# Performance work log

Hardware: AMD Instinct MI355X
Metric: run time of the kernel (lower is better)

Reference implementation:

```python
import jax, jax.numpy as jnp
from jax import lax
import numpy as np

K = 48          # dim_embedding_key
PAST = 20
FUT = 40
N = 65536       # total surrounding-agent nodes
E = 1048576     # edges
B = 1           # batch (structurally forced to 1 by the original code)


def conv1d_relu(x, w, b):
    # x: [B, 2, T], w: [K, 2, 3], padding=1 -> relu(Conv1d)
    y = lax.conv_general_dilated(x, w, (1,), ((1, 1),),
                                 dimension_numbers=('NCH', 'OIH', 'NCH'))
    return jax.nn.relu(y + b[None, :, None])


def gru_cell(xt, h, Wih, Whh, bih, bhh):
    gi = xt @ Wih.T + bih
    gh = h @ Whh.T + bhh
    ir, iz, inn = jnp.split(gi, 3, axis=-1)
    hr, hz, hn = jnp.split(gh, 3, axis=-1)
    r = jax.nn.sigmoid(ir + hr)
    z = jax.nn.sigmoid(iz + hz)
    n = jnp.tanh(inn + r * hn)
    return (1 - z) * n + z * h


def gru_last(x, Wih, Whh, bih, bhh):
    # x: [Nb, T, Din]; returns final hidden state [Nb, H] (torch GRU, h0 = 0)
    h0 = jnp.zeros((x.shape[0], Whh.shape[1]), x.dtype)
    def step(h, xt):
        h2 = gru_cell(xt, h, Wih, Whh, bih, bhh)
        return h2, None
    hT, _ = lax.scan(step, h0, jnp.swapaxes(x, 0, 1))
    return hT


def gcn_conv(x, row, col, w, W, b, n):
    # PyG GCNConv(normalize=True): add self loops (weight 1), symmetric norm,
    # x @ W.T, gather at source `row`, scatter-add at target `col`, + bias.
    loop = jnp.arange(n)
    row = jnp.concatenate([row, loop])
    col = jnp.concatenate([col, loop])
    w = jnp.concatenate([w, jnp.ones((n,), w.dtype)])
    deg = jax.ops.segment_sum(w, col, num_segments=n)
    dinv = jnp.where(deg > 0, lax.rsqrt(jnp.where(deg > 0, deg, 1.0)), 0.0)
    norm = dinv[row] * w * dinv[col]
    xw = x @ W.T
    msg = xw[row] * norm[:, None]
    return jax.ops.segment_sum(msg, col, num_segments=n) + b


def forward(past, future, x, edge_index, edge_weight,
            conv_past_w, conv_past_b, conv_fut_w, conv_fut_b,
            enc_past_Wih, enc_past_Whh, enc_past_bih, enc_past_bhh,
            enc_fut_Wih, enc_fut_Whh, enc_fut_bih, enc_fut_bhh,
            dec_Wih, dec_Whh, dec_bih, dec_bhh,
            fc_w, fc_b, gcn1_w, gcn1_b, gcn2_w, gcn2_b):
    present0 = past[:, -1, :2]                                  # [B, 2]

    # --- surrounding agents: conv1d + GRU encoder over all N nodes ---
    inter_past = jnp.swapaxes(x.reshape(-1, PAST, 2), 1, 2)     # [N, 2, T]
    story_embed = jnp.swapaxes(conv1d_relu(inter_past, conv_past_w, conv_past_b), 1, 2)
    state_past = gru_last(story_embed, enc_past_Wih, enc_past_Whh, enc_past_bih, enc_past_bhh)  # [N, K]

    # --- GCN interaction (edge_weight nonempty branch); dropout is eval-mode identity ---
    ei = edge_index.reshape(2, -1)
    ew = edge_weight.reshape(-1)
    x1 = jax.nn.relu(gcn_conv(state_past, ei[0], ei[1], ew, gcn1_w, gcn1_b, N))
    x1 = gcn_conv(x1, ei[0], ei[1], ew, gcn2_w, gcn2_b, N)
    interact_past = x1[0].reshape(B, -1)                        # [B, K] (B == 1)

    # --- ego past / future encoders ---
    past_embed = jnp.swapaxes(conv1d_relu(jnp.swapaxes(past, 1, 2), conv_past_w, conv_past_b), 1, 2)
    fut_embed = jnp.swapaxes(conv1d_relu(jnp.swapaxes(future, 1, 2), conv_fut_w, conv_fut_b), 1, 2)
    target_past = gru_last(past_embed, enc_past_Wih, enc_past_Whh, enc_past_bih, enc_past_bhh)   # [B, K]
    state_fut = gru_last(fut_embed, enc_fut_Wih, enc_fut_Whh, enc_fut_bih, enc_fut_bhh)          # [B, K]

    state_conc = jnp.concatenate([interact_past, target_past, state_fut], axis=-1)               # [B, 3K]

    zeros_in = jnp.zeros_like(state_conc)
    def step(carry, i):
        h, present = carry
        inp = jnp.where(i == 0, state_conc, zeros_in)
        h = gru_cell(inp, h, dec_Wih, dec_Whh, dec_bih, dec_bhh)
        coords = present + h @ fc_w.T + fc_b
        return (h, coords), coords
    (_, _), coords_seq = lax.scan(step, (jnp.zeros((B, 3 * K), past.dtype), present0), jnp.arange(FUT))
    return jnp.swapaxes(coords_seq, 0, 1)                        # [B, FUT, 2]


def setup_inputs() -> dict:
    ks = jax.random.split(jax.random.key(0), 32)
    def p(k, shape, s=0.1):
        return jax.random.normal(k, shape, jnp.float32) * s
    inp = {
        'past': p(ks[0], (B, PAST, 2), 1.0),
        'future': p(ks[1], (B, FUT, 2), 1.0),
        'x': p(ks[2], (N, PAST, 2), 1.0),
        'edge_index': jax.random.randint(ks[3], (1, 2, E), 0, N, jnp.int32),
        'edge_weight': jax.random.uniform(ks[4], (1, E), jnp.float32),
        'conv_past_w': p(ks[5], (K, 2, 3)), 'conv_past_b': p(ks[6], (K,)),
        'conv_fut_w': p(ks[7], (K, 2, 3)), 'conv_fut_b': p(ks[8], (K,)),
        'enc_past_Wih': p(ks[9], (3 * K, K)), 'enc_past_Whh': p(ks[10], (3 * K, K)),
        'enc_past_bih': p(ks[11], (3 * K,)), 'enc_past_bhh': p(ks[12], (3 * K,)),
        'enc_fut_Wih': p(ks[13], (3 * K, K)), 'enc_fut_Whh': p(ks[14], (3 * K, K)),
        'enc_fut_bih': p(ks[15], (3 * K,)), 'enc_fut_bhh': p(ks[16], (3 * K,)),
        'dec_Wih': p(ks[17], (9 * K, 3 * K)), 'dec_Whh': p(ks[18], (9 * K, 3 * K)),
        'dec_bih': p(ks[19], (9 * K,)), 'dec_bhh': p(ks[20], (9 * K,)),
        'fc_w': p(ks[21], (2, 3 * K)), 'fc_b': p(ks[22], (2,)),
        'gcn1_w': p(ks[23], (K, K)), 'gcn1_b': p(ks[24], (K,)),
        'gcn2_w': p(ks[25], (K, K)), 'gcn2_b': p(ks[26], (K,)),
    }
    return inp


def reference(past, future, x, edge_index, edge_weight,
              conv_past_w, conv_past_b, conv_fut_w, conv_fut_b,
              enc_past_Wih, enc_past_Whh, enc_past_bih, enc_past_bhh,
              enc_fut_Wih, enc_fut_Whh, enc_fut_bih, enc_fut_bhh,
              dec_Wih, dec_Whh, dec_bih, dec_bhh,
              fc_w, fc_b, gcn1_w, gcn1_b, gcn2_w, gcn2_b):
    return forward(past, future, x, edge_index, edge_weight,
                   conv_past_w, conv_past_b, conv_fut_w, conv_fut_b,
                   enc_past_Wih, enc_past_Whh, enc_past_bih, enc_past_bhh,
                   enc_fut_Wih, enc_fut_Whh, enc_fut_bih, enc_fut_bhh,
                   dec_Wih, dec_Whh, dec_bih, dec_bhh,
                   fc_w, fc_b, gcn1_w, gcn1_b, gcn2_w, gcn2_b)
```

## Files before the change

kernel.cpp:

```cpp
#include <hip/hip_runtime.h>
#include <math.h>

#define NN 65536
#define NE 1048576
#define KH 48
#define G3 144
#define DEGB 512
#define PREPB 15

#define CAP_L1 8192
#define CAP_S1 4096
#define CAP_E2 65536
#define CAP_S2 8192

#define OFF_MARK1  0u
#define OFF_MARK2  262144u
#define OFF_CNT    524288u
#define OFF_L1R    524352u
#define OFF_L1W    557120u
#define OFF_S1G    589888u
#define OFF_E2R    606272u
#define OFF_E2S    868416u
#define OFF_E2W    1130560u
#define OFF_S2     1392704u
#define OFF_DEG2   1425472u
#define OFF_STATE  1458240u
#define OFF_X1     3031104u
#define OFF_TPSF   3817536u
#define OFF_WHH16  3818048u
#define OFF_GI0P   3942464u
#define OFF_GIP    3944192u
#define OFF_GIF    3955712u

typedef _Float16 h2_t __attribute__((ext_vector_type(2)));
typedef _Float16 h4_t __attribute__((ext_vector_type(4)));

__device__ __forceinline__ float sigmf(float x) { return 1.0f / (1.0f + expf(-x)); }

#if __has_builtin(__builtin_amdgcn_fdot2)
__device__ __forceinline__ float fdot2f(h2_t a, h2_t b, float c) {
    return __builtin_amdgcn_fdot2(a, b, c, false);
}
#else
__device__ __forceinline__ float fdot2f(h2_t a, h2_t b, float c) {
    return c + (float)a.x * (float)b.x + (float)a.y * (float)b.y;
}
#endif

__global__ void k_edges1(const int* ei, const float* ew,
                         int* mark1, unsigned* cnt, int* l1r, float* l1w,
                         const float* past, const float* future,
                         const float* cpw, const float* cpb,
                         const float* cfw, const float* cfb,
                         const float* epWih, const float* epbih,
                         const float* efWih, const float* efbih,
                         float* giP, float* giF) {
    if (blockIdx.x >= NE / 4 / 256) {
        int p = blockIdx.x - NE / 4 / 256;
        const float* xs; const float* cw; const float* cb;
        const float* Wih; const float* bih; float* gout;
        int T, s0;
        if (p < 5) { xs = past;   cw = cpw; cb = cpb; Wih = epWih; bih = epbih;
                     gout = giP; T = 20; s0 = p * 4; }
        else       { xs = future; cw = cfw; cb = cfb; Wih = efWih; bih = efbih;
                     gout = giF; T = 40; s0 = (p - 5) * 4; }
        __shared__ __align__(16) float s_x[80];
        __shared__ __align__(16) float s_e[4 * KH];
        int t = threadIdx.x;
        if (t < T * 2) s_x[t] = xs[t];
        __syncthreads();
        for (int idx = t; idx < 4 * KH; idx += 256) {
            int lt = idx / KH;
            int k = idx - lt * KH;
            int tt = s0 + lt;
            float acc = cb[k];
#pragma unroll
            for (int d = 0; d < 3; ++d) {
                int tau = tt + d - 1;
                if (tau >= 0 && tau < T) {
                    acc += cw[k * 6 + d] * s_x[tau * 2 + 0];
                    acc += cw[k * 6 + 3 + d] * s_x[tau * 2 + 1];
                }
            }
            s_e[lt * KH + k] = fmaxf(acc, 0.0f);
        }
        __syncthreads();
        for (int idx = t; idx < 4 * G3; idx += 256) {
            int lt = idx / G3;
            int row = idx - lt * G3;
            const float4* wp = reinterpret_cast<const float4*>(Wih + row * KH);
            const float4* em = reinterpret_cast<const float4*>(s_e + lt * KH);
            float g = bih[row];
#pragma unroll
            for (int j = 0; j < 12; ++j) {
                float4 w4 = wp[j]; float4 e4 = em[j];
                g += w4.x * e4.x + w4.y * e4.y + w4.z * e4.z + w4.w * e4.w;
            }
            gout[(s0 + lt) * G3 + row] = g;
        }
        return;
    }
    int q = blockIdx.x * blockDim.x + threadIdx.x;
    if (q >= NE / 4) return;
    if (q == 0) mark1[0] = 1;
    int4 c4 = reinterpret_cast<const int4*>(ei + NE)[q];
    int e = q * 4;
    int cc[4] = {c4.x, c4.y, c4.z, c4.w};
#pragma unroll
    for (int j = 0; j < 4; ++j) {
        if (cc[j] == 0) {
            int r = ei[e + j];
            float w = ew[e + j];
            unsigned s = atomicAdd(&cnt[0], 1u);
            if (s < CAP_L1) { l1r[s] = r; l1w[s] = w; }
            mark1[r] = 1;
        }
    }
}

__global__ void k_compact1(int* mark1, int* mark2, unsigned* cnt,
                           int* e2r, int* e2s, float* e2w, int* s1g,
                           float* x1, const float* g1b) {
    int i = blockIdx.x * blockDim.x + threadIdx.x;
    if (i >= NN) return;
    if (mark1[i]) {
        unsigned s = atomicAdd(&cnt[1], 1u);
        if (s < CAP_S1) {
            mark1[i] = (int)s + 1;
            mark2[i] = 1;
            s1g[s] = i;
            unsigned t = atomicAdd(&cnt[2], 1u);
            if (t < CAP_E2) { e2r[t] = i; e2s[t] = (int)s; e2w[t] = 1.0f; }
            for (int k = 0; k < KH; ++k) x1[s * KH + k] = g1b[k];
        } else {
            mark1[i] = 0;
        }
    }
}

__global__ void k_edges2(const int* ei, const float* ew,
                         const int* mark1, int* mark2, unsigned* cnt,
                         int* e2r, int* e2s, float* e2w) {
    int q = blockIdx.x * blockDim.x + threadIdx.x;
    if (q >= NE / 4) return;
    int4 c4 = reinterpret_cast<const int4*>(ei + NE)[q];
    int e = q * 4;
    int cc[4] = {c4.x, c4.y, c4.z, c4.w};
#pragma unroll
    for (int j = 0; j < 4; ++j) {
        int m = mark1[cc[j]];
        if (m > 0) {
            int r = ei[e + j];
            float w = ew[e + j];
            unsigned s = atomicAdd(&cnt[2], 1u);
            if (s < CAP_E2) { e2r[s] = r; e2s[s] = m - 1; e2w[s] = w; }
            mark2[r] = 1;
        }
    }
}

__global__ void k_compact2(int* mark2, unsigned* cnt, int* s2, float* deg2) {
    int i = blockIdx.x * blockDim.x + threadIdx.x;
    if (i >= NN) return;
    if (mark2[i]) {
        unsigned s = atomicAdd(&cnt[3], 1u);
        if (s < CAP_S2) { s2[s] = i; mark2[i] = (int)s + 1; deg2[s] = 1.0f; }
        else mark2[i] = 0;
    }
}

__device__ void gru_seq(const float* xseq, int T,
                        const float* cw, const float* cb,
                        const float* Wih, const float* Whh,
                        const float* bih, const float* bhh,
                        float* out48,
                        float* s_x, float* s_embed, float* s_giA,
                        float* s_h ) {
    int t = threadIdx.x;
    int nt = blockDim.x;
    for (int i = t; i < T * 2; i += nt) s_x[i] = xseq[i];
    __syncthreads();
    for (int idx = t; idx < T * KH; idx += nt) {
        int tt = idx / KH;
        int k = idx - tt * KH;
        float acc = cb[k];
#pragma unroll
        for (int d = 0; d < 3; ++d) {
            int tau = tt + d - 1;
            if (tau >= 0 && tau < T) {
                acc += cw[k * 6 + d] * s_x[tau * 2 + 0];
                acc += cw[k * 6 + 3 + d] * s_x[tau * 2 + 1];
            }
        }
        s_embed[tt * KH + k] = fmaxf(acc, 0.0f);
    }
    __syncthreads();
    for (int idx = t; idx < T * G3; idx += nt) {
        int step = idx / G3;
        int row = idx - step * G3;
        const float4* wp = reinterpret_cast<const float4*>(Wih + row * KH);
        const float4* em = reinterpret_cast<const float4*>(s_embed + step * KH);
        float g = bih[row];
#pragma unroll
        for (int j = 0; j < 12; ++j) {
            float4 w4 = wp[j]; float4 e4 = em[j];
            g += w4.x * e4.x + w4.y * e4.y + w4.z * e4.z + w4.w * e4.w;
        }
        s_giA[idx] = g;
    }
    int k = t >> 1, hf = t & 1;
    float4 wr[18];
    float bh0 = 0.0f, bh1 = 0.0f, bh2 = 0.0f;
    if (t < 96) {
#pragma unroll
        for (int g = 0; g < 3; ++g) {
            const float4* q = reinterpret_cast<const float4*>(
                Whh + (g * KH + k) * KH + hf * 24);
#pragma unroll
            for (int j = 0; j < 6; ++j) wr[g * 6 + j] = q[j];
        }
        if (hf == 0) { bh0 = bhh[k]; bh1 = bhh[KH + k]; bh2 = bhh[2 * KH + k]; }
    }
    if (t < KH) s_h[t] = 0.0f;
    float hk = 0.0f;
    for (int step = 0; step < T; ++step) {
        __syncthreads();
        int cur = step & 1, nxt = cur ^ 1;
        if (t < 96) {
            const float4* hp = reinterpret_cast<const float4*>(s_h + cur * KH)
                               + hf * 6;
            float a0 = bh0, a1 = bh1, a2 = bh2;
#pragma unroll
            for (int j = 0; j < 6; ++j) {
                float4 hv = hp[j];
                float4 w0 = wr[j], w1 = wr[6 + j], w2 = wr[12 + j];
                a0 += w0.x * hv.x + w0.y * hv.y + w0.z * hv.z + w0.w * hv.w;
                a1 += w1.x * hv.x + w1.y * hv.y + w1.z * hv.z + w1.w * hv.w;
                a2 += w2.x * hv.x + w2.y * hv.y + w2.z * hv.z + w2.w * hv.w;
            }
            a0 += __shfl_xor(a0, 1);
            a1 += __shfl_xor(a1, 1);
            a2 += __shfl_xor(a2, 1);
            if (hf == 0) {
                const float* gi = s_giA + step * G3;
                float r = sigmf(gi[k] + a0);
                float z = sigmf(gi[KH + k] + a1);
                float n = tanhf(gi[2 * KH + k] + r * a2);
                hk = (1.0f - z) * n + z * hk;
                s_h[nxt * KH + k] = hk;
            }
        }
    }
    __syncthreads();
    if (t < KH) out48[t] = s_h[(T & 1) * KH + t];
}

__device__ void gru_rec(const float* giA , int T,
                        const float* Whh, const float* bhh,
                        float* out48, float* s_h ) {
    int t = threadIdx.x;
    int k = t >> 1, hf = t & 1;
    float4 wr[18];
    float bh0 = 0.0f, bh1 = 0.0f, bh2 = 0.0f;
    if (t < 96) {
#pragma unroll
        for (int g = 0; g < 3; ++g) {
            const float4* q = reinterpret_cast<const float4*>(
                Whh + (g * KH + k) * KH + hf * 24);
#pragma unroll
            for (int j = 0; j < 6; ++j) wr[g * 6 + j] = q[j];
        }
        if (hf == 0) { bh0 = bhh[k]; bh1 = bhh[KH + k]; bh2 = bhh[2 * KH + k]; }
    }
    if (t < KH) s_h[t] = 0.0f;
    float hk = 0.0f;
    for (int step = 0; step < T; ++step) {
        __syncthreads();
        int cur = step & 1, nxt = cur ^ 1;
        if (t < 96) {
            const float4* hp = reinterpret_cast<const float4*>(s_h + cur * KH)
                               + hf * 6;
            float a0 = bh0, a1 = bh1, a2 = bh2;
#pragma unroll
            for (int j = 0; j < 6; ++j) {
                float4 hv = hp[j];
                float4 w0 = wr[j], w1 = wr[6 + j], w2 = wr[12 + j];
                a0 += w0.x * hv.x + w0.y * hv.y + w0.z * hv.z + w0.w * hv.w;
                a1 += w1.x * hv.x + w1.y * hv.y + w1.z * hv.z + w1.w * hv.w;
                a2 += w2.x * hv.x + w2.y * hv.y + w2.z * hv.z + w2.w * hv.w;
            }
            a0 += __shfl_xor(a0, 1);
            a1 += __shfl_xor(a1, 1);
            a2 += __shfl_xor(a2, 1);
            if (hf == 0) {
                const float* gi = giA + step * G3;
                float r = sigmf(gi[k] + a0);
                float z = sigmf(gi[KH + k] + a1);
                float n = tanhf(gi[2 * KH + k] + r * a2);
                hk = (1.0f - z) * n + z * hk;
                s_h[nxt * KH + k] = hk;
            }
        }
    }
    __syncthreads();
    if (t < KH) out48[t] = s_h[(T & 1) * KH + t];
}

__global__ __launch_bounds__(192, 2) void k_gru(
    const float* x, const float* cpw, const float* cpb,
    const float* epWih, const float* epWhh, const float* epbih, const float* epbhh,
    const float* efWhh, const float* efbhh,
    const float* giP, const float* giF,
    const int* ei, const float* ew, const int* mark2, float* deg2,
    const int* s2, const unsigned* cnt, float* state, float* tpsf) {
    if (blockIdx.x < DEGB) {
        int per = NE / DEGB;
        int lo = blockIdx.x * per;
        for (int e = lo + threadIdx.x; e < lo + per; e += blockDim.x) {
            int c = ei[NE + e];
            int m = mark2[c];
            if (m > 0) atomicAdd(&deg2[m - 1], ew[e]);
        }
        return;
    }
    __shared__ __align__(16) float s_x[80];
    __shared__ __align__(16) float s_embed[40 * KH];
    __shared__ __align__(16) float s_giA[40 * G3];
    __shared__ __align__(16) float s_h[2 * KH];
    if (blockIdx.x == DEGB) {
        gru_rec(giP, 20, epWhh, epbhh, tpsf, s_h);
        return;
    }
    if (blockIdx.x == DEGB + 1) {
        gru_rec(giF, 40, efWhh, efbhh, tpsf + 64, s_h);
        return;
    }
    int b0 = blockIdx.x - (DEGB + 2);
    int nw = gridDim.x - (DEGB + 2);
    int cnt2 = (int)min(cnt[3], (unsigned)CAP_S2);
    for (int b = b0; b < cnt2; b += nw) {
        int node = s2[b];
        gru_seq(x + (size_t)node * 40, 20, cpw, cpb, epWih, epWhh, epbih, epbhh,
                state + (size_t)b * KH, s_x, s_embed, s_giA, s_h);
    }
}

__global__ void k_acc1(const unsigned* cnt, const int* e2r, const int* e2s,
                       const float* e2w, const int* mark2, const float* deg2,
                       const int* s1g, const float* state,
                       const float* W1, float* x1,
                       const float* dWhh, const float* dWih,
                       const float* dbih, const float* tpsf,
                       _Float16* whh16, float* gi0p) {
    if (blockIdx.x < 64) {
        int id = blockIdx.x * blockDim.x + threadIdx.x;
        if (id < 27 * 576) {
            int c = id / 576, t = id - c * 576;
            int k = t >> 2, q = t & 3;
            int g = c / 9, u = c - g * 9;
            const float* src = dWhh + (size_t)(g * G3 + k) * G3 + q * 36 + 4 * u;
            float4 f = *reinterpret_cast<const float4*>(src);
            h2_t a, b;
            a.x = (_Float16)f.x; a.y = (_Float16)f.y;
            b.x = (_Float16)f.z; b.y = (_Float16)f.w;
            h2_t* o = reinterpret_cast<h2_t*>(whh16);
            o[2 * id + 0] = a;
            o[2 * id + 1] = b;
            return;
        }
        int row = id - 27 * 576;
        if (row < 432) {
            const float* wr = dWih + (size_t)row * G3;
            float acc = dbih[row];
#pragma unroll
            for (int m = 0; m < 48; ++m) acc += wr[48 + m] * tpsf[m];
#pragma unroll
            for (int m = 0; m < 48; ++m) acc += wr[96 + m] * tpsf[64 + m];
            gi0p[row] = acc;
        }
        return;
    }
    int nE = (int)min(cnt[2], (unsigned)CAP_E2);
    int total = nE * KH;
    int stride = (gridDim.x - 64) * blockDim.x;
    for (int idx = (blockIdx.x - 64) * blockDim.x + threadIdx.x; idx < total;
         idx += stride) {
        int e = idx / KH;
        int k = idx - e * KH;
        int row = e2r[e];
        int s2i = mark2[row] - 1;
        if (s2i < 0) continue;
        int cglob = s1g[e2s[e]];
        int cs2 = mark2[cglob] - 1;
        float norm = e2w[e] * rsqrtf(deg2[s2i] * deg2[cs2]);
        const float* sp = state + (size_t)s2i * KH;
        const float* wp = W1 + k * KH;
        float acc = 0.0f;
#pragma unroll
        for (int m = 0; m < KH; ++m) acc += sp[m] * wp[m];
        atomicAdd(&x1[e2s[e] * KH + k], acc * norm);
    }
}

__global__ __launch_bounds__(640, 1) void k_dec(
    const unsigned* cnt, const int* l1r, const float* l1w,
    const int* mark1, const int* mark2, const float* deg2, const float* x1,
    const float* W2, const float* b2, const float* tpsf, const float* past,
    const float* dWih, const _Float16* whh16, const float* gi0p,
    const float* dbih, const float* dbhh,
    const float* fcw, const float* fcb, float* out) {
    __shared__ __align__(16) float s_conc[G3];
    __shared__ __align__(16) _Float16 s_h16[2][G3];
    __shared__ __align__(16) float s_hf[2][G3];
    int t = threadIdx.x;
    if (t < 48) s_conc[t] = b2[t];
    else if (t < 96) s_conc[t] = tpsf[t - 48];
    else if (t < 144) s_conc[t] = tpsf[64 + t - 96];
    if (t < G3) {
        s_h16[0][t] = (_Float16)0.0f;
        s_hf[0][t] = 0.0f;
    }
    __syncthreads();
    int cl1 = (int)min(cnt[0], (unsigned)CAP_L1);
    float dinv0 = rsqrtf(deg2[mark2[0] - 1]);
    int items = (cl1 + 1) * KH;
    for (int idx = t; idx < items; idx += blockDim.x) {
        int e = idx / KH;
        int k = idx - e * KH;
        int row; float norm;
        if (e == cl1) { row = 0; norm = dinv0 * dinv0; }
        else {
            row = l1r[e];
            int rs2 = mark2[row] - 1;
            if (rs2 < 0) continue;
            norm = l1w[e] * rsqrtf(deg2[rs2]) * dinv0;
        }
        int s1 = mark1[row] - 1;
        if (s1 < 0) continue;
        const float* xp = x1 + (size_t)s1 * KH;
        const float* wp = W2 + k * KH;
        float acc = 0.0f;
#pragma unroll
        for (int m = 0; m < KH; ++m) acc += fmaxf(xp[m], 0.0f) * wp[m];
        atomicAdd(&s_conc[k], acc * norm);
    }
    int k = t >> 2, q = t & 3;
    h2_t wh[54];
    float bh[3] = {0.0f, 0.0f, 0.0f};
    float bi[3] = {0.0f, 0.0f, 0.0f};
    if (t < 576) {
        const h4_t* wp = reinterpret_cast<const h4_t*>(whh16);
#pragma unroll
        for (int c = 0; c < 27; ++c) {
            h4_t v = wp[c * 576 + t];
            wh[2 * c] = __builtin_shufflevector(v, v, 0, 1);
            wh[2 * c + 1] = __builtin_shufflevector(v, v, 2, 3);
        }
        if (q == 0) {
#pragma unroll
            for (int g = 0; g < 3; ++g) {
                bh[g] = dbhh[g * G3 + k];
                bi[g] = dbih[g * G3 + k];
            }
        }
    }
    float fw0[3] = {0, 0, 0}, fw1[3] = {0, 0, 0};
    float fcb0 = 0.0f, fcb1 = 0.0f, pres0 = 0.0f, pres1 = 0.0f;
    if (t >= 576) {
        int lane = t - 576;
#pragma unroll
        for (int j = 0; j < 3; ++j) {
            int m = lane + 64 * j;
            if (m < G3) { fw0[j] = fcw[m]; fw1[j] = fcw[G3 + m]; }
        }
        if (lane == 0) {
            fcb0 = fcb[0]; fcb1 = fcb[1];
            pres0 = past[38]; pres1 = past[39];
        }
    }
    __syncthreads();
    float gi0[3] = {0.0f, 0.0f, 0.0f};
    if (t < 576) {
#pragma unroll
        for (int g = 0; g < 3; ++g) {
            float acc = 0.0f;
            if (q == 0) {
                const float4* p = reinterpret_cast<const float4*>(
                    dWih + (size_t)(g * G3 + k) * G3);
                const float4* cc = reinterpret_cast<const float4*>(s_conc);
#pragma unroll
                for (int j = 0; j < 9; ++j) {
                    float4 w4 = p[j]; float4 c4 = cc[j];
                    acc += w4.x * c4.x + w4.y * c4.y + w4.z * c4.z + w4.w * c4.w;
                }
            } else if (q == 1) {
                const float4* p = reinterpret_cast<const float4*>(
                    dWih + (size_t)(g * G3 + k) * G3 + 36);
                const float4* cc = reinterpret_cast<const float4*>(s_conc + 36);
#pragma unroll
                for (int j = 0; j < 3; ++j) {
                    float4 w4 = p[j]; float4 c4 = cc[j];
                    acc += w4.x * c4.x + w4.y * c4.y + w4.z * c4.z + w4.w * c4.w;
                }
            }
            acc += __shfl_xor(acc, 1);
            acc += __shfl_xor(acc, 2);
            gi0[g] = acc + gi0p[g * G3 + k];
        }
    }
    float hk = 0.0f;
    for (int i = 0; i < 40; ++i) {
        __syncthreads();
        int cur = i & 1, nxt = cur ^ 1;
        if (t < 576) {
            const h4_t* hp = reinterpret_cast<const h4_t*>(&s_h16[cur][0]) + q * 9;
            float a0 = bh[0], a1 = bh[1], a2 = bh[2];
#pragma unroll
            for (int j = 0; j < 9; ++j) {
                h4_t hv = hp[j];
                h2_t lo = __builtin_shufflevector(hv, hv, 0, 1);
                h2_t hi = __builtin_shufflevector(hv, hv, 2, 3);
                a0 = fdot2f(wh[2 * j], lo, a0);
                a1 = fdot2f(wh[18 + 2 * j], lo, a1);
                a2 = fdot2f(wh[36 + 2 * j], lo, a2);
                a0 = fdot2f(wh[2 * j + 1], hi, a0);
                a1 = fdot2f(wh[18 + 2 * j + 1], hi, a1);
                a2 = fdot2f(wh[36 + 2 * j + 1], hi, a2);
            }
            a0 += __shfl_xor(a0, 1); a0 += __shfl_xor(a0, 2);
            a1 += __shfl_xor(a1, 1); a1 += __shfl_xor(a1, 2);
            a2 += __shfl_xor(a2, 1); a2 += __shfl_xor(a2, 2);
            if (q == 0) {
                float gr = ((i == 0) ? gi0[0] : bi[0]) + a0;
                float gz = ((i == 0) ? gi0[1] : bi[1]) + a1;
                float gn = ((i == 0) ? gi0[2] : bi[2]);
                float r = sigmf(gr);
                float z = sigmf(gz);
                float n = tanhf(gn + r * a2);
                hk = (1.0f - z) * n + z * hk;
                s_h16[nxt][k] = (_Float16)hk;
                s_hf[nxt][k] = hk;
            }
        } else if (i >= 1) {
            int lane = t - 576;
            const float* hsrc = s_hf[cur];
            float p0 = 0.0f, p1 = 0.0f;
#pragma unroll
            for (int j = 0; j < 3; ++j) {
                int m = lane + 64 * j;
                if (m < G3) { float h = hsrc[m]; p0 += h * fw0[j]; p1 += h * fw1[j]; }
            }
#pragma unroll
            for (int off = 32; off > 0; off >>= 1) {
                p0 += __shfl_down(p0, off);
                p1 += __shfl_down(p1, off);
            }
            if (lane == 0) {
                pres0 += p0 + fcb0; pres1 += p1 + fcb1;
                out[(i - 1) * 2 + 0] = pres0;
                out[(i - 1) * 2 + 1] = pres1;
            }
        }
    }
    __syncthreads();
    if (t >= 576) {
        int lane = t - 576;
        const float* hsrc = s_hf[0];
        float p0 = 0.0f, p1 = 0.0f;
#pragma unroll
        for (int j = 0; j < 3; ++j) {
            int m = lane + 64 * j;
            if (m < G3) { float h = hsrc[m]; p0 += h * fw0[j]; p1 += h * fw1[j]; }
        }
#pragma unroll
        for (int off = 32; off > 0; off >>= 1) {
            p0 += __shfl_down(p0, off);
            p1 += __shfl_down(p1, off);
        }
        if (lane == 0) {
            pres0 += p0 + fcb0; pres1 += p1 + fcb1;
            out[39 * 2 + 0] = pres0;
            out[39 * 2 + 1] = pres1;
        }
    }
}

extern "C" void kernel_launch(void* const* d_in, const int* in_sizes, int n_in,
                              void* d_out, int out_size, void* d_ws, size_t ws_size,
                              hipStream_t stream) {
    (void)in_sizes; (void)n_in; (void)out_size; (void)ws_size;
    const float* past   = (const float*)d_in[0];
    const float* future = (const float*)d_in[1];
    const float* x      = (const float*)d_in[2];
    const int*   ei     = (const int*)d_in[3];
    const float* ew     = (const float*)d_in[4];
    const float* cpw    = (const float*)d_in[5];
    const float* cpb    = (const float*)d_in[6];
    const float* cfw    = (const float*)d_in[7];
    const float* cfb    = (const float*)d_in[8];
    const float* epWih  = (const float*)d_in[9];
    const float* epWhh  = (const float*)d_in[10];
    const float* epbih  = (const float*)d_in[11];
    const float* epbhh  = (const float*)d_in[12];
    const float* efWih  = (const float*)d_in[13];
    const float* efWhh  = (const float*)d_in[14];
    const float* efbih  = (const float*)d_in[15];
    const float* efbhh  = (const float*)d_in[16];
    const float* dWih   = (const float*)d_in[17];
    const float* dWhh   = (const float*)d_in[18];
    const float* dbih   = (const float*)d_in[19];
    const float* dbhh   = (const float*)d_in[20];
    const float* fcw    = (const float*)d_in[21];
    const float* fcb    = (const float*)d_in[22];
    const float* g1w    = (const float*)d_in[23];
    const float* g1b    = (const float*)d_in[24];
    const float* g2w    = (const float*)d_in[25];
    const float* g2b    = (const float*)d_in[26];

    char* ws = (char*)d_ws;
    int*      mark1 = (int*)(ws + OFF_MARK1);
    int*      mark2 = (int*)(ws + OFF_MARK2);
    unsigned* cnt   = (unsigned*)(ws + OFF_CNT);
    int*      l1r   = (int*)(ws + OFF_L1R);
    float*    l1w   = (float*)(ws + OFF_L1W);
    int*      s1g   = (int*)(ws + OFF_S1G);
    int*      e2r   = (int*)(ws + OFF_E2R);
    int*      e2s   = (int*)(ws + OFF_E2S);
    float*    e2w   = (float*)(ws + OFF_E2W);
    int*      s2    = (int*)(ws + OFF_S2);
    float*    deg2  = (float*)(ws + OFF_DEG2);
    float*    state = (float*)(ws + OFF_STATE);
    float*    x1    = (float*)(ws + OFF_X1);
    float*    tpsf  = (float*)(ws + OFF_TPSF);
    _Float16* whh16 = (_Float16*)(ws + OFF_WHH16);
    float*    gi0p  = (float*)(ws + OFF_GI0P);
    float*    giP   = (float*)(ws + OFF_GIP);
    float*    giF   = (float*)(ws + OFF_GIF);

    hipMemsetAsync(ws, 0, 524352, stream);
    k_edges1<<<NE / 4 / 256 + PREPB, 256, 0, stream>>>(
        ei, ew, mark1, cnt, l1r, l1w,
        past, future, cpw, cpb, cfw, cfb,
        epWih, epbih, efWih, efbih, giP, giF);
    k_compact1<<<NN / 256, 256, 0, stream>>>(mark1, mark2, cnt, e2r, e2s, e2w, s1g, x1, g1b);
    k_edges2<<<NE / 4 / 256, 256, 0, stream>>>(ei, ew, mark1, mark2, cnt, e2r, e2s, e2w);
    k_compact2<<<NN / 256, 256, 0, stream>>>(mark2, cnt, s2, deg2);
    k_gru<<<DEGB + 2 + 512, 192, 0, stream>>>(x, cpw, cpb, epWih, epWhh, epbih, epbhh,
                                              efWhh, efbhh, giP, giF,
                                              ei, ew, mark2, deg2,
                                              s2, cnt, state, tpsf);
    k_acc1<<<64 + 128, 256, 0, stream>>>(cnt, e2r, e2s, e2w, mark2, deg2, s1g,
                                         state, g1w, x1,
                                         dWhh, dWih, dbih, tpsf, whh16, gi0p);
    k_dec<<<1, 640, 0, stream>>>(cnt, l1r, l1w, mark1, mark2, deg2, x1, g2w, g2b,
                                 tpsf, past, dWih, whh16, gi0p, dbih, dbhh, fcw, fcb,
                                 (float*)d_out);
}
```

Before: 224.7 us.

## Pre-stage decoder weights in coalesced layouts and use fast exp-based activations

The decoder Whh fp16 staging is repacked so the single-block decoder loads 8 halves per thread instead of 4, cutting the number of load instructions. The first-step input projection (dWih columns 0..47) is also pre-staged into a thread-major float4 layout, so all four lanes of a quad share the work with coalesced loads instead of lanes 0 and 1 doing uneven strided loops. sigmoid and tanh now use __expf-based fast forms in the encoder and decoder GRUs, which loses some accuracy. The staging kernel gets extra blocks for the new copy.

```diff
diff --git a/kernel.cpp b/kernel.cpp
--- a/kernel.cpp
+++ b/kernel.cpp
@@ -7,6 +7,7 @@
 #define G3 144
 #define DEGB 512
 #define PREPB 15
+#define STAGEB 83
 
 #define CAP_L1 8192
 #define CAP_S1 4096
@@ -28,14 +29,20 @@
 #define OFF_X1     3031104u
 #define OFF_TPSF   3817536u
 #define OFF_WHH16  3818048u
-#define OFF_GI0P   3942464u
-#define OFF_GIP    3944192u
-#define OFF_GIF    3955712u
+#define OFF_GI0P   3947072u
+#define OFF_GIP    3948800u
+#define OFF_GIF    3960320u
+#define OFF_DWH4   3983360u
 
 typedef _Float16 h2_t __attribute__((ext_vector_type(2)));
 typedef _Float16 h4_t __attribute__((ext_vector_type(4)));
-
-__device__ __forceinline__ float sigmf(float x) { return 1.0f / (1.0f + expf(-x)); }
+typedef _Float16 h8_t __attribute__((ext_vector_type(8)));
+
+__device__ __forceinline__ float sigmf(float x) { return 1.0f / (1.0f + __expf(-x)); }
+__device__ __forceinline__ float tanhfast(float x) {
+    float e = __expf(2.0f * x);
+    return 1.0f - 2.0f / (e + 1.0f);
+}
 
 #if __has_builtin(__builtin_amdgcn_fdot2)
 __device__ __forceinline__ float fdot2f(h2_t a, h2_t b, float c) {
@@ -245,7 +252,7 @@
                 const float* gi = s_giA + step * G3;
                 float r = sigmf(gi[k] + a0);
                 float z = sigmf(gi[KH + k] + a1);
-                float n = tanhf(gi[2 * KH + k] + r * a2);
+                float n = tanhfast(gi[2 * KH + k] + r * a2);
                 hk = (1.0f - z) * n + z * hk;
                 s_h[nxt * KH + k] = hk;
             }
@@ -296,7 +303,7 @@
                 const float* gi = giA + step * G3;
                 float r = sigmf(gi[k] + a0);
                 float z = sigmf(gi[KH + k] + a1);
-                float n = tanhf(gi[2 * KH + k] + r * a2);
+                float n = tanhfast(gi[2 * KH + k] + r * a2);
                 hk = (1.0f - z) * n + z * hk;
                 s_h[nxt * KH + k] = hk;
             }
@@ -351,8 +358,8 @@
                        const float* W1, float* x1,
                        const float* dWhh, const float* dWih,
                        const float* dbih, const float* tpsf,
-                       _Float16* whh16, float* gi0p) {
-    if (blockIdx.x < 64) {
+                       _Float16* whh16, float* dwh4, float* gi0p) {
+    if (blockIdx.x < STAGEB) {
         int id = blockIdx.x * blockDim.x + threadIdx.x;
         if (id < 27 * 576) {
             int c = id / 576, t = id - c * 576;
@@ -363,12 +370,23 @@
             h2_t a, b;
             a.x = (_Float16)f.x; a.y = (_Float16)f.y;
             b.x = (_Float16)f.z; b.y = (_Float16)f.w;
+            int pid = ((c >> 1) * 576 + t) * 2 + (c & 1);
             h2_t* o = reinterpret_cast<h2_t*>(whh16);
-            o[2 * id + 0] = a;
-            o[2 * id + 1] = b;
+            o[2 * pid + 0] = a;
+            o[2 * pid + 1] = b;
             return;
         }
-        int row = id - 27 * 576;
+        if (id < 27 * 576 + 9 * 576) {
+            int id2 = id - 27 * 576;
+            int c = id2 / 576, t = id2 - c * 576;
+            int k = t >> 2, q = t & 3;
+            int g = c / 3, j = c - g * 3;
+            const float* src = dWih + (size_t)(g * G3 + k) * G3 + q * 12 + 4 * j;
+            reinterpret_cast<float4*>(dwh4)[id2] =
+                *reinterpret_cast<const float4*>(src);
+            return;
+        }
+        int row = id - (27 * 576 + 9 * 576);
         if (row < 432) {
             const float* wr = dWih + (size_t)row * G3;
             float acc = dbih[row];
@@ -382,8 +400,8 @@
     }
     int nE = (int)min(cnt[2], (unsigned)CAP_E2);
     int total = nE * KH;
-    int stride = (gridDim.x - 64) * blockDim.x;
-    for (int idx = (blockIdx.x - 64) * blockDim.x + threadIdx.x; idx < total;
+    int stride = (gridDim.x - STAGEB) * blockDim.x;
+    for (int idx = (blockIdx.x - STAGEB) * blockDim.x + threadIdx.x; idx < total;
          idx += stride) {
         int e = idx / KH;
         int k = idx - e * KH;
@@ -406,7 +424,7 @@
     const unsigned* cnt, const int* l1r, const float* l1w,
     const int* mark1, const int* mark2, const float* deg2, const float* x1,
     const float* W2, const float* b2, const float* tpsf, const float* past,
-    const float* dWih, const _Float16* whh16, const float* gi0p,
+    const _Float16* whh16, const float* dwh4, const float* gi0p,
     const float* dbih, const float* dbhh,
     const float* fcw, const float* fcb, float* out) {
     __shared__ __align__(16) float s_conc[G3];
@@ -449,13 +467,22 @@
     float bh[3] = {0.0f, 0.0f, 0.0f};
     float bi[3] = {0.0f, 0.0f, 0.0f};
     if (t < 576) {
-        const h4_t* wp = reinterpret_cast<const h4_t*>(whh16);
-#pragma unroll
-        for (int c = 0; c < 27; ++c) {
-            h4_t v = wp[c * 576 + t];
-            wh[2 * c] = __builtin_shufflevector(v, v, 0, 1);
-            wh[2 * c + 1] = __builtin_shufflevector(v, v, 2, 3);
-        }
+        const h8_t* wp8 = reinterpret_cast<const h8_t*>(whh16);
+#pragma unroll
+        for (int c2 = 0; c2 < 13; ++c2) {
+            h8_t v = wp8[c2 * 576 + t];
+            int c0 = 2 * c2, c1 = 2 * c2 + 1;
+            int g0 = c0 / 9, u0 = c0 - g0 * 9;
+            int g1 = c1 / 9, u1 = c1 - g1 * 9;
+            wh[g0 * 18 + 2 * u0]     = __builtin_shufflevector(v, v, 0, 1);
+            wh[g0 * 18 + 2 * u0 + 1] = __builtin_shufflevector(v, v, 2, 3);
+            wh[g1 * 18 + 2 * u1]     = __builtin_shufflevector(v, v, 4, 5);
+            wh[g1 * 18 + 2 * u1 + 1] = __builtin_shufflevector(v, v, 6, 7);
+        }
+        const h4_t* wp4 = reinterpret_cast<const h4_t*>(whh16);
+        h4_t v26 = wp4[(13 * 576 + t) * 2];
+        wh[2 * 18 + 2 * 8]     = __builtin_shufflevector(v26, v26, 0, 1);
+        wh[2 * 18 + 2 * 8 + 1] = __builtin_shufflevector(v26, v26, 2, 3);
         if (q == 0) {
 #pragma unroll
             for (int g = 0; g < 3; ++g) {
@@ -481,28 +508,17 @@
     __syncthreads();
     float gi0[3] = {0.0f, 0.0f, 0.0f};
     if (t < 576) {
+        const float4* dp = reinterpret_cast<const float4*>(dwh4);
+        const float4* cc = reinterpret_cast<const float4*>(s_conc) + q * 3;
+        float4 c0 = cc[0], c1 = cc[1], c2v = cc[2];
 #pragma unroll
         for (int g = 0; g < 3; ++g) {
-            float acc = 0.0f;
-            if (q == 0) {
-                const float4* p = reinterpret_cast<const float4*>(
-                    dWih + (size_t)(g * G3 + k) * G3);
-                const float4* cc = reinterpret_cast<const float4*>(s_conc);
-#pragma unroll
-                for (int j = 0; j < 9; ++j) {
-                    float4 w4 = p[j]; float4 c4 = cc[j];
-                    acc += w4.x * c4.x + w4.y * c4.y + w4.z * c4.z + w4.w * c4.w;
-                }
-            } else if (q == 1) {
-                const float4* p = reinterpret_cast<const float4*>(
-                    dWih + (size_t)(g * G3 + k) * G3 + 36);
-                const float4* cc = reinterpret_cast<const float4*>(s_conc + 36);
-#pragma unroll
-                for (int j = 0; j < 3; ++j) {
-                    float4 w4 = p[j]; float4 c4 = cc[j];
-                    acc += w4.x * c4.x + w4.y * c4.y + w4.z * c4.z + w4.w * c4.w;
-                }
-            }
+            float4 w0 = dp[(g * 3 + 0) * 576 + t];
+            float4 w1 = dp[(g * 3 + 1) * 576 + t];
+            float4 w2 = dp[(g * 3 + 2) * 576 + t];
+            float acc = w0.x * c0.x + w0.y * c0.y + w0.z * c0.z + w0.w * c0.w;
+            acc += w1.x * c1.x + w1.y * c1.y + w1.z * c1.z + w1.w * c1.w;
+            acc += w2.x * c2v.x + w2.y * c2v.y + w2.z * c2v.z + w2.w * c2v.w;
             acc += __shfl_xor(acc, 1);
             acc += __shfl_xor(acc, 2);
             gi0[g] = acc + gi0p[g * G3 + k];
@@ -536,7 +552,7 @@
                 float gn = ((i == 0) ? gi0[2] : bi[2]);
                 float r = sigmf(gr);
                 float z = sigmf(gz);
-                float n = tanhf(gn + r * a2);
+                float n = tanhfast(gn + r * a2);
                 hk = (1.0f - z) * n + z * hk;
                 s_h16[nxt][k] = (_Float16)hk;
                 s_hf[nxt][k] = hk;
@@ -636,6 +652,7 @@
     float*    gi0p  = (float*)(ws + OFF_GI0P);
     float*    giP   = (float*)(ws + OFF_GIP);
     float*    giF   = (float*)(ws + OFF_GIF);
+    float*    dwh4  = (float*)(ws + OFF_DWH4);
 
     hipMemsetAsync(ws, 0, 524352, stream);
     k_edges1<<<NE / 4 / 256 + PREPB, 256, 0, stream>>>(
@@ -649,10 +666,11 @@
                                               efWhh, efbhh, giP, giF,
                                               ei, ew, mark2, deg2,
                                               s2, cnt, state, tpsf);
-    k_acc1<<<64 + 128, 256, 0, stream>>>(cnt, e2r, e2s, e2w, mark2, deg2, s1g,
-                                         state, g1w, x1,
-                                         dWhh, dWih, dbih, tpsf, whh16, gi0p);
+    k_acc1<<<STAGEB + 128, 256, 0, stream>>>(cnt, e2r, e2s, e2w, mark2, deg2, s1g,
+                                             state, g1w, x1,
+                                             dWhh, dWih, dbih, tpsf,
+                                             whh16, dwh4, gi0p);
     k_dec<<<1, 640, 0, stream>>>(cnt, l1r, l1w, mark1, mark2, deg2, x1, g2w, g2b,
-                                 tpsf, past, dWih, whh16, gi0p, dbih, dbhh, fcw, fcb,
+                                 tpsf, past, whh16, dwh4, gi0p, dbih, dbhh, fcw, fcb,
                                  (float*)d_out);
 }
```

Result: faster. 217.4 us (-3.3%).
